# Kernel optimization log

Measured on AMD Instinct MI355X. Metric: run time of the kernel, lower is better.

Reference implementation:

```python
import jax, jax.numpy as jnp
import numpy as np

B, LONG, SHORT, D, NH, HD = 512, 1000, 50, 64, 4, 16
NUM_ITEMS, TOPK = 100000, 50
NBUCKETS, HASHL, HASHD = 1024, 4, 16  # NOTE: 4 hash layers of D//4 so concat matches item_dim (source default 3 is a shape bug)


def lin(x, w, b):
    return x @ w.T + b


def ln(x, g, b):
    m = x.mean(-1, keepdims=True)
    v = ((x - m) ** 2).mean(-1, keepdims=True)
    return (x - m) / jnp.sqrt(v + 1e-5) * g + b


def setup_inputs() -> dict:
    key = jax.random.key(0)
    ks = jax.random.split(key, 24)
    rn = lambda i, s: jax.random.normal(ks[i], s, jnp.float32) * 0.02
    emb = rn(0, (NUM_ITEMS + 1, D)).at[0].set(0.0)  # padding_idx=0 row zeroed
    return dict(
        user_features=jax.random.normal(ks[1], (B, D), jnp.float32),
        target_item_id=jax.random.randint(ks[2], (B,), 0, NUM_ITEMS + 1),
        short_hist_ids=jax.random.randint(ks[3], (B, SHORT), 0, NUM_ITEMS + 1),
        long_hist_ids=jax.random.randint(ks[4], (B, LONG), 0, NUM_ITEMS + 1),
        item_emb=emb,
        tproj_w=rn(5, (D, D)), tproj_b=jnp.zeros((D,), jnp.float32),
        attn_w1=rn(6, (64, 3 * D)), attn_b1=jnp.zeros((64,), jnp.float32),
        attn_w2=rn(7, (1, 64)), attn_b2=jnp.zeros((1,), jnp.float32),
        hash_emb=rn(8, (HASHL, NBUCKETS, HASHD)),
        sdim_w=rn(9, (D, D)), sdim_b=jnp.zeros((D,), jnp.float32),
        tf_qkv_w=rn(10, (2, 3 * D, D)), tf_qkv_b=jnp.zeros((2, 3 * D), jnp.float32),
        tf_out_w=rn(11, (2, D, D)), tf_out_b=jnp.zeros((2, D), jnp.float32),
        tf_ln1_g=jnp.ones((2, D), jnp.float32), tf_ln1_b=jnp.zeros((2, D), jnp.float32),
        tf_ff1_w=rn(12, (2, 2 * D, D)), tf_ff1_b=jnp.zeros((2, 2 * D), jnp.float32),
        tf_ff2_w=rn(13, (2, D, 2 * D)), tf_ff2_b=jnp.zeros((2, D), jnp.float32),
        tf_ln2_g=jnp.ones((2, D), jnp.float32), tf_ln2_b=jnp.zeros((2, D), jnp.float32),
        fus_w1=rn(14, (256, 4 * D)), fus_b1=jnp.zeros((256,), jnp.float32),
        fus_w2=rn(15, (128, 256)), fus_b2=jnp.zeros((128,), jnp.float32),
        fus_w3=rn(16, (1, 128)), fus_b3=jnp.zeros((1,), jnp.float32),
    )


def sim_forward(user_features, item_emb, tproj_w, tproj_b, attn_w1, attn_b1,
                attn_w2, attn_b2, hash_emb, sdim_w, sdim_b, tf_qkv_w, tf_qkv_b,
                tf_out_w, tf_out_b, tf_ln1_g, tf_ln1_b, tf_ff1_w, tf_ff1_b,
                tf_ff2_w, tf_ff2_b, tf_ln2_g, tf_ln2_b, fus_w1, fus_b1, fus_w2,
                fus_b2, fus_w3, fus_b3, target_item_id, short_hist_ids, long_hist_ids):
    # target projection
    target_emb = lin(item_emb[target_item_id], tproj_w, tproj_b)         # [B,D]
    # ---- hard search over long history ----
    long_emb = item_emb[long_hist_ids]                                    # [B,L,D]
    t = jnp.broadcast_to(target_emb[:, None, :], long_emb.shape)
    cc = jnp.concatenate([t, long_emb, long_emb * t], axis=-1)            # [B,L,3D]
    scores = lin(jax.nn.relu(lin(cc, attn_w1, attn_b1)), attn_w2, attn_b2)[..., 0]
    attn = jax.nn.softmax(scores, axis=-1)                                # [B,L]
    top_w, top_i = jax.lax.top_k(attn, TOPK)
    top_w = jax.nn.softmax(top_w, axis=-1)
    top_e = jnp.take_along_axis(long_emb, top_i[..., None], axis=1)       # [B,K,D]
    hard_repr = (top_w[..., None] * top_e).sum(axis=1)                    # [B,D]
    # ---- SDIM soft search ----
    bucket = long_hist_ids % NBUCKETS
    h = hash_emb[:, bucket].mean(axis=2)                                  # [HL,B,HD]
    hash_repr = jnp.moveaxis(h, 0, 1).reshape(h.shape[1], HASHL * HASHD)  # [B,D]
    soft_repr = lin(hash_repr + long_emb.mean(axis=1), sdim_w, sdim_b)    # [B,D]
    # ---- BST transformer over short history (post-norm, relu, dropout=eval) ----
    x = item_emb[short_hist_ids]                                          # [B,S,D]
    for l in range(2):
        qkv = lin(x, tf_qkv_w[l], tf_qkv_b[l])
        q, k, v = jnp.split(qkv, 3, axis=-1)
        q = q.reshape(B, SHORT, NH, HD); k = k.reshape(B, SHORT, NH, HD); v = v.reshape(B, SHORT, NH, HD)
        sc = jnp.einsum('bqhd,bkhd->bhqk', q, k) / np.sqrt(HD).astype(np.float32)
        a = jax.nn.softmax(sc, axis=-1)
        o = jnp.einsum('bhqk,bkhd->bqhd', a, v).reshape(B, SHORT, D)
        x = ln(x + lin(o, tf_out_w[l], tf_out_b[l]), tf_ln1_g[l], tf_ln1_b[l])
        f = lin(jax.nn.relu(lin(x, tf_ff1_w[l], tf_ff1_b[l])), tf_ff2_w[l], tf_ff2_b[l])
        x = ln(x + f, tf_ln2_g[l], tf_ln2_b[l])
    bst_repr = x.mean(axis=1)                                             # [B,D]
    # ---- fusion MLP ----
    combined = jnp.concatenate([user_features, hard_repr, soft_repr, bst_repr], axis=-1)
    hdn = jax.nn.relu(lin(combined, fus_w1, fus_b1))
    hdn = jax.nn.relu(lin(hdn, fus_w2, fus_b2))
    return lin(hdn, fus_w3, fus_b3)[..., 0]                               # [B]


def reference(user_features, target_item_id, short_hist_ids, long_hist_ids,
              item_emb, tproj_w, tproj_b, attn_w1, attn_b1, attn_w2, attn_b2,
              hash_emb, sdim_w, sdim_b, tf_qkv_w, tf_qkv_b, tf_out_w, tf_out_b,
              tf_ln1_g, tf_ln1_b, tf_ff1_w, tf_ff1_b, tf_ff2_w, tf_ff2_b,
              tf_ln2_g, tf_ln2_b, fus_w1, fus_b1, fus_w2, fus_b2, fus_w3, fus_b3):
    return sim_forward(user_features, item_emb, tproj_w, tproj_b, attn_w1, attn_b1,
                       attn_w2, attn_b2, hash_emb, sdim_w, sdim_b, tf_qkv_w, tf_qkv_b,
                       tf_out_w, tf_out_b, tf_ln1_g, tf_ln1_b, tf_ff1_w, tf_ff1_b,
                       tf_ff2_w, tf_ff2_b, tf_ln2_g, tf_ln2_b, fus_w1, fus_b1,
                       fus_w2, fus_b2, fus_w3, fus_b3, target_item_id,
                       short_hist_ids, long_hist_ids)
```

## Files before the change

kernel.cpp:

```cpp
#include <hip/hip_runtime.h>
#include <math.h>

#define NB 512
#define LONGN 1000
#define SHORTN 50
#define TOPKN 50
#define HALFN 500
#define NG 8
#define EROW 72
#define BROW 72
#define F1ROW 136

typedef __attribute__((ext_vector_type(8))) short bf16x8;
typedef __attribute__((ext_vector_type(4))) float f32x4;

__device__ __forceinline__ float dot4(float4 a, float4 b) {
  return a.x*b.x + a.y*b.y + a.z*b.z + a.w*b.w;
}

template<int N>
__device__ __forceinline__ float dotN(const float* w, const float* x) {
  const float4* w4 = (const float4*)w;
  const float4* x4 = (const float4*)x;
  float a0 = 0.f, a1 = 0.f, a2 = 0.f, a3 = 0.f;
  #pragma unroll
  for (int k = 0; k < N/4; k += 4) {
    a0 += dot4(w4[k],   x4[k]);
    a1 += dot4(w4[k+1], x4[k+1]);
    a2 += dot4(w4[k+2], x4[k+2]);
    a3 += dot4(w4[k+3], x4[k+3]);
  }
  return (a0 + a1) + (a2 + a3);
}

__device__ __forceinline__ float wave_sum(float v) {
  #pragma unroll
  for (int off = 32; off > 0; off >>= 1) v += __shfl_xor(v, off);
  return v;
}
__device__ __forceinline__ float wave_max(float v) {
  #pragma unroll
  for (int off = 32; off > 0; off >>= 1) v = fmaxf(v, __shfl_xor(v, off));
  return v;
}

__device__ __forceinline__ unsigned short f2bf(float x) {
  unsigned u = __float_as_uint(x);
  return (unsigned short)((u + 0x7fffu + ((u >> 16) & 1u)) >> 16);
}

__global__ __launch_bounds__(256, 3) void hard_scores_kernel(
    const int* __restrict__ target_item_id,
    const int* __restrict__ long_hist_ids,
    const float* __restrict__ item_emb,
    const float* __restrict__ tproj_w, const float* __restrict__ tproj_b,
    const float* __restrict__ attn_w1, const float* __restrict__ attn_b1,
    const float* __restrict__ attn_w2, const float* __restrict__ attn_b2,
    const float* __restrict__ hash_emb,
    float* __restrict__ scores_ws, float* __restrict__ partA,
    float* __restrict__ partH)
{
  __shared__ __align__(16) short Abf[64*EROW];
  __shared__ __align__(16) short Ebuf[2][64*EROW];
  __shared__ __align__(16) float tv[64];
  __shared__ __align__(16) float te[64];
  __shared__ __align__(16) float2 cw[64];
  __shared__ int idsL[HALFN];
  __shared__ __align__(16) float redE[4*64];

  const int bid = blockIdx.x;
  const int b = bid >> 1, half = bid & 1;
  const int base = half * HALFN;
  const int tid = threadIdx.x;
  const int wid = tid >> 6, lane = tid & 63;

  if (tid < 64) tv[tid] = item_emb[target_item_id[b]*64 + tid];
  for (int l = tid; l < HALFN; l += 256) idsL[l] = long_hist_ids[b*LONGN + base + l];
  __syncthreads();
  if (tid < 64) te[tid] = tproj_b[tid] + dotN<64>(tproj_w + tid*64, tv);
  __syncthreads();
  if (tid < 64) {
    float c = attn_b1[tid] + dotN<64>(attn_w1 + tid*192, te);
    cw[tid] = make_float2(c, attn_w2[tid]);
  }
  for (int idx = tid; idx < 4096; idx += 256) {
    int i = idx >> 6, j = idx & 63;
    Abf[i*EROW + j] = (short)f2bf(attn_w1[i*192 + 64 + j] + attn_w1[i*192 + 128 + j]*te[j]);
  }
  __syncthreads();

  bf16x8 a00,a01,a10,a11,a20,a21,a30,a31;
  {
    const short* ap = Abf + (lane & 15)*EROW + ((lane >> 4) << 3);
    a00 = *(const bf16x8*)(ap +  0*EROW);  a01 = *(const bf16x8*)(ap +  0*EROW + 32);
    a10 = *(const bf16x8*)(ap + 16*EROW);  a11 = *(const bf16x8*)(ap + 16*EROW + 32);
    a20 = *(const bf16x8*)(ap + 32*EROW);  a21 = *(const bf16x8*)(ap + 32*EROW + 32);
    a30 = *(const bf16x8*)(ap + 48*EROW);  a31 = *(const bf16x8*)(ap + 48*EROW + 32);
  }

  const float b2s = attn_b2[0];
  const int it_g = tid >> 2;
  const int dimg = (tid & 3) * 16;

  float4 sE0 = {0,0,0,0}, sE1 = {0,0,0,0}, sE2 = {0,0,0,0}, sE3 = {0,0,0,0};

  {
    const float4* ep = (const float4*)(item_emb + (size_t)idsL[it_g]*64 + dimg);
    float4 r0 = ep[0], r1 = ep[1], r2 = ep[2], r3 = ep[3];
    sE0.x+=r0.x; sE0.y+=r0.y; sE0.z+=r0.z; sE0.w+=r0.w;
    sE1.x+=r1.x; sE1.y+=r1.y; sE1.z+=r1.z; sE1.w+=r1.w;
    sE2.x+=r2.x; sE2.y+=r2.y; sE2.z+=r2.z; sE2.w+=r2.w;
    sE3.x+=r3.x; sE3.y+=r3.y; sE3.z+=r3.z; sE3.w+=r3.w;
    bf16x8 w0, w1;
    w0[0]=(short)f2bf(r0.x); w0[1]=(short)f2bf(r0.y); w0[2]=(short)f2bf(r0.z); w0[3]=(short)f2bf(r0.w);
    w0[4]=(short)f2bf(r1.x); w0[5]=(short)f2bf(r1.y); w0[6]=(short)f2bf(r1.z); w0[7]=(short)f2bf(r1.w);
    w1[0]=(short)f2bf(r2.x); w1[1]=(short)f2bf(r2.y); w1[2]=(short)f2bf(r2.z); w1[3]=(short)f2bf(r2.w);
    w1[4]=(short)f2bf(r3.x); w1[5]=(short)f2bf(r3.y); w1[6]=(short)f2bf(r3.z); w1[7]=(short)f2bf(r3.w);
    short* dst = &Ebuf[0][it_g*EROW + dimg];
    *(bf16x8*)dst = w0;  *(bf16x8*)(dst + 8) = w1;
  }
  __syncthreads();

  int buf = 0;
  for (int g = 0; g < NG; ++g) {
    float4 r0={0,0,0,0}, r1={0,0,0,0}, r2={0,0,0,0}, r3={0,0,0,0};
    const bool more = (g + 1 < NG);
    if (more) {
      const int gi = (g+1)*64 + it_g;
      if (gi < HALFN) {
        const float4* ep = (const float4*)(item_emb + (size_t)idsL[gi]*64 + dimg);
        r0 = ep[0]; r1 = ep[1]; r2 = ep[2]; r3 = ep[3];
      }
    }

    f32x4 acc0={0,0,0,0}, acc1={0,0,0,0}, acc2={0,0,0,0}, acc3={0,0,0,0};
    {
      const short* ep = &Ebuf[buf][(wid*16 + (lane & 15))*EROW + ((lane >> 4) << 3)];
      bf16x8 b0 = *(const bf16x8*)(ep);
      bf16x8 b1 = *(const bf16x8*)(ep + 32);
      acc0 = __builtin_amdgcn_mfma_f32_16x16x32_bf16(a00, b0, acc0, 0, 0, 0);
      acc0 = __builtin_amdgcn_mfma_f32_16x16x32_bf16(a01, b1, acc0, 0, 0, 0);
      acc1 = __builtin_amdgcn_mfma_f32_16x16x32_bf16(a10, b0, acc1, 0, 0, 0);
      acc1 = __builtin_amdgcn_mfma_f32_16x16x32_bf16(a11, b1, acc1, 0, 0, 0);
      acc2 = __builtin_amdgcn_mfma_f32_16x16x32_bf16(a20, b0, acc2, 0, 0, 0);
      acc2 = __builtin_amdgcn_mfma_f32_16x16x32_bf16(a21, b1, acc2, 0, 0, 0);
      acc3 = __builtin_amdgcn_mfma_f32_16x16x32_bf16(a30, b0, acc3, 0, 0, 0);
      acc3 = __builtin_amdgcn_mfma_f32_16x16x32_bf16(a31, b1, acc3, 0, 0, 0);
    }
    float p = 0.f;
    {
      const int rbase = (lane >> 4) << 2;
      #pragma unroll
      for (int r = 0; r < 4; ++r) {
        float2 c0 = cw[ 0 + rbase + r];
        float2 c1 = cw[16 + rbase + r];
        float2 c2 = cw[32 + rbase + r];
        float2 c3 = cw[48 + rbase + r];
        p += c0.y * fmaxf(acc0[r] + c0.x, 0.f);
        p += c1.y * fmaxf(acc1[r] + c1.x, 0.f);
        p += c2.y * fmaxf(acc2[r] + c2.x, 0.f);
        p += c3.y * fmaxf(acc3[r] + c3.x, 0.f);
      }
    }
    p += __shfl_xor(p, 16);
    p += __shfl_xor(p, 32);
    if (lane < 16) {
      const int gi = g*64 + wid*16 + lane;
      if (gi < HALFN) scores_ws[b*LONGN + base + gi] = b2s + p;
    }

    if (more) {
      sE0.x+=r0.x; sE0.y+=r0.y; sE0.z+=r0.z; sE0.w+=r0.w;
      sE1.x+=r1.x; sE1.y+=r1.y; sE1.z+=r1.z; sE1.w+=r1.w;
      sE2.x+=r2.x; sE2.y+=r2.y; sE2.z+=r2.z; sE2.w+=r2.w;
      sE3.x+=r3.x; sE3.y+=r3.y; sE3.z+=r3.z; sE3.w+=r3.w;
      bf16x8 w0, w1;
      w0[0]=(short)f2bf(r0.x); w0[1]=(short)f2bf(r0.y); w0[2]=(short)f2bf(r0.z); w0[3]=(short)f2bf(r0.w);
      w0[4]=(short)f2bf(r1.x); w0[5]=(short)f2bf(r1.y); w0[6]=(short)f2bf(r1.z); w0[7]=(short)f2bf(r1.w);
      w1[0]=(short)f2bf(r2.x); w1[1]=(short)f2bf(r2.y); w1[2]=(short)f2bf(r2.z); w1[3]=(short)f2bf(r2.w);
      w1[4]=(short)f2bf(r3.x); w1[5]=(short)f2bf(r3.y); w1[6]=(short)f2bf(r3.z); w1[7]=(short)f2bf(r3.w);
      short* dst = &Ebuf[buf ^ 1][it_g*EROW + dimg];
      *(bf16x8*)dst = w0;  *(bf16x8*)(dst + 8) = w1;
    }
    __syncthreads();
    buf ^= 1;
  }

  {
    float* red = (float*)&Ebuf[0][0];
    const int b17 = tid * 17;
    red[b17+ 0]=sE0.x; red[b17+ 1]=sE0.y; red[b17+ 2]=sE0.z; red[b17+ 3]=sE0.w;
    red[b17+ 4]=sE1.x; red[b17+ 5]=sE1.y; red[b17+ 6]=sE1.z; red[b17+ 7]=sE1.w;
    red[b17+ 8]=sE2.x; red[b17+ 9]=sE2.y; red[b17+10]=sE2.z; red[b17+11]=sE2.w;
    red[b17+12]=sE3.x; red[b17+13]=sE3.y; red[b17+14]=sE3.z; red[b17+15]=sE3.w;
    __syncthreads();
    if (tid < 64) {
      const int dg = tid >> 4, dw = tid & 15;
      float s = 0.f;
      for (int j = 0; j < 64; ++j) s += red[(j*4 + dg)*17 + dw];
      partA[bid*64 + tid] = s;
    }
  }

  {
    const int hl = lane >> 4, dd = lane & 15;
    const float* hb = hash_emb + hl*1024*16 + dd;
    float accH = 0.f;
    for (int l = wid; l < HALFN; l += 4)
      accH += hb[(idsL[l] & 1023)*16];
    redE[wid*64 + lane] = accH;
  }
  __syncthreads();
  if (wid == 0)
    partH[bid*64 + lane] = redE[lane] + redE[64+lane] + redE[128+lane] + redE[192+lane];
}

__global__ __launch_bounds__(256) void hard_finish_kernel(
    const int* __restrict__ long_hist_ids,
    const float* __restrict__ item_emb,
    const float* __restrict__ sdim_w, const float* __restrict__ sdim_b,
    const float* __restrict__ scores_ws,
    const float* __restrict__ partA, const float* __restrict__ partH,
    float* __restrict__ hard_out, float* __restrict__ soft_out)
{
  __shared__ __align__(16) float scores[LONGN];
  __shared__ int   idsL[LONGN];
  __shared__ __align__(16) unsigned long long kv[1024];
  __shared__ __align__(16) float redE[4*64];
  __shared__ __align__(16) float vecbuf[64];
  __shared__ float redV[4];
  __shared__ float selV[TOPKN];
  __shared__ int   selI[TOPKN];

  const int b = blockIdx.x;
  const int tid = threadIdx.x;
  const int wid = tid >> 6, lane = tid & 63;

  for (int l = tid; l < LONGN; l += 256) {
    scores[l] = scores_ws[b*LONGN + l];
    idsL[l] = long_hist_ids[b*LONGN + l];
  }
  __syncthreads();

  if (tid < 64)
    vecbuf[tid] = (partA[(2*b)*64 + tid] + partA[(2*b+1)*64 + tid]
                 + partH[(2*b)*64 + tid] + partH[(2*b+1)*64 + tid]) * (1.f/1000.f);
  __syncthreads();
  if (tid < 64)
    soft_out[b*64 + tid] = sdim_b[tid] + dotN<64>(sdim_w + tid*64, vecbuf);

  float mx = -INFINITY;
  for (int l = tid; l < LONGN; l += 256) mx = fmaxf(mx, scores[l]);
  mx = wave_max(mx);
  if (lane == 0) redV[wid] = mx;
  __syncthreads();
  mx = fmaxf(fmaxf(redV[0], redV[1]), fmaxf(redV[2], redV[3]));
  __syncthreads();
  float sm = 0.f;
  for (int l = tid; l < LONGN; l += 256) {
    float a = expf(scores[l] - mx);
    scores[l] = a;
    sm += a;
  }
  sm = wave_sum(sm);
  if (lane == 0) redV[wid] = sm;
  __syncthreads();
  {
    const float inv = 1.f / (redV[0] + redV[1] + redV[2] + redV[3]);
    for (int l = tid; l < LONGN; l += 256) scores[l] *= inv;
  }
  __syncthreads();

  for (int l = tid; l < 1024; l += 256) {
    if (l < LONGN) {
      unsigned vb = __float_as_uint(scores[l]);
      kv[l] = ((unsigned long long)(~vb) << 32) | (unsigned)l;
    } else {
      kv[l] = 0xFFFFFFFFFFFFFFFFull;
    }
  }
  __syncthreads();

  for (int k = 2; k <= 1024; k <<= 1) {
    for (int j = k >> 1; j > 0; j >>= 1) {
      #pragma unroll 2
      for (int p = tid; p < 512; p += 256) {
        const int i = ((p & ~(j-1)) << 1) | (p & (j-1));
        const int m = i + j;
        const bool up = ((i & k) == 0);
        unsigned long long a = kv[i], c = kv[m];
        if ((a > c) == up) { kv[i] = c; kv[m] = a; }
      }
      __syncthreads();
    }
  }

  if (tid < TOPKN) {
    unsigned long long key = kv[tid];
    selI[tid] = (int)(unsigned)(key & 0xFFFFFFFFu);
    selV[tid] = __uint_as_float(~(unsigned)(key >> 32));
  }
  __syncthreads();

  if (wid == 0) {
    float v = (lane < TOPKN) ? selV[lane] : -INFINITY;
    float m2 = wave_max(v);
    float e = (lane < TOPKN) ? expf(v - m2) : 0.f;
    float s2 = wave_sum(e);
    if (lane < TOPKN) selV[lane] = e / s2;
  }
  __syncthreads();

  float accR = 0.f;
  for (int r = wid; r < TOPKN; r += 4)
    accR += selV[r] * item_emb[idsL[selI[r]]*64 + lane];
  redE[wid*64 + lane] = accR;
  __syncthreads();
  if (wid == 0)
    hard_out[b*64 + lane] = redE[lane] + redE[64+lane] + redE[128+lane] + redE[192+lane];
}

__global__ __launch_bounds__(256) void bst_prep_kernel(
    const float* __restrict__ qkv_w, const float* __restrict__ out_w,
    const float* __restrict__ ff1_w, const float* __restrict__ ff2_w,
    short* __restrict__ wF)
{
  const int t = blockIdx.x*256 + threadIdx.x;
  if (t >= 8192) return;
  const int fid = t >> 6, lane = t & 63;
  const int n16 = lane & 15, k8 = (lane >> 4) * 8;
  const float* src;
  if (fid < 48)      { int f=fid,    l=f/24, r=f%24, nt=r>>1, kc=r&1;
    src = qkv_w + l*12288 + (nt*16+n16)*64 + kc*32 + k8; }
  else if (fid < 64) { int f=fid-48, l=f>>3, r=f&7,  nt=r>>1, kc=r&1;
    src = out_w + l*4096 + (nt*16+n16)*64 + kc*32 + k8; }
  else if (fid < 96) { int f=fid-64, l=f>>4, r=f&15, nt=r>>1, kc=r&1;
    src = ff1_w + l*8192 + (nt*16+n16)*64 + kc*32 + k8; }
  else               { int f=fid-96, l=f>>4, r=f&15, nt=r>>2, kc=r&3;
    src = ff2_w + l*8192 + (nt*16+n16)*128 + kc*32 + k8; }
  short* dst = wF + fid*512 + lane*8;
  #pragma unroll
  for (int j = 0; j < 8; ++j) dst[j] = (short)f2bf(src[j]);
}

__global__ __launch_bounds__(256) void bst_kernel(
    const int* __restrict__ short_ids, const float* __restrict__ item_emb,
    const short* __restrict__ wF,
    const float* __restrict__ qkv_b, const float* __restrict__ out_b,
    const float* __restrict__ ln1_g, const float* __restrict__ ln1_b,
    const float* __restrict__ ff1_b, const float* __restrict__ ff2_b,
    const float* __restrict__ ln2_g, const float* __restrict__ ln2_b,
    float* __restrict__ bst_out)
{
  __shared__ __align__(16) float xf[SHORTN*64];
  __shared__ __align__(16) short xbf[64*BROW];
  __shared__ __align__(16) float qf[SHORTN*68];
  __shared__ __align__(16) float arena[SHORTN*132];
  __shared__ __align__(16) short obf[64*BROW];

  short* f1bf = (short*)arena;

  const int b = blockIdx.x, tid = threadIdx.x;
  const int wid = tid >> 6, lane = tid & 63;
  const int n16 = lane & 15;
  const int kg8 = (lane >> 4) << 3;
  const int mrow = (lane >> 4) << 2;

  for (int idx = tid; idx < SHORTN*64; idx += 256) {
    int s = idx >> 6, j = idx & 63;
    float v = item_emb[short_ids[b*SHORTN + s]*64 + j];
    xf[idx] = v;
    xbf[s*BROW + j] = (short)f2bf(v);
  }
  for (int idx = tid; idx < 14*BROW; idx += 256) {
    xbf[50*BROW + idx] = 0;
    obf[50*BROW + idx] = 0;
  }
  __syncthreads();

  for (int l = 0; l < 2; ++l) {
    {
      const short* ap = xbf + n16*BROW + kg8;
      bf16x8 A00 = *(const bf16x8*)(ap);            bf16x8 A01 = *(const bf16x8*)(ap + 32);
      bf16x8 A10 = *(const bf16x8*)(ap + 16*BROW);  bf16x8 A11 = *(const bf16x8*)(ap + 16*BROW + 32);
      bf16x8 A20 = *(const bf16x8*)(ap + 32*BROW);  bf16x8 A21 = *(const bf16x8*)(ap + 32*BROW + 32);
      bf16x8 A30 = *(const bf16x8*)(ap + 48*BROW);  bf16x8 A31 = *(const bf16x8*)(ap + 48*BROW + 32);
      #pragma unroll
      for (int t = 0; t < 3; ++t) {
        const int nt = wid*3 + t;
        const short* bp = wF + (size_t)(l*24 + nt*2)*512 + lane*8;
        bf16x8 B0 = *(const bf16x8*)(bp);
        bf16x8 B1 = *(const bf16x8*)(bp + 512);
        f32x4 c0={0,0,0,0}, c1={0,0,0,0}, c2={0,0,0,0}, c3={0,0,0,0};
        c0 = __builtin_amdgcn_mfma_f32_16x16x32_bf16(A00, B0, c0, 0,0,0);
        c0 = __builtin_amdgcn_mfma_f32_16x16x32_bf16(A01, B1, c0, 0,0,0);
        c1 = __builtin_amdgcn_mfma_f32_16x16x32_bf16(A10, B0, c1, 0,0,0);
        c1 = __builtin_amdgcn_mfma_f32_16x16x32_bf16(A11, B1, c1, 0,0,0);
        c2 = __builtin_amdgcn_mfma_f32_16x16x32_bf16(A20, B0, c2, 0,0,0);
        c2 = __builtin_amdgcn_mfma_f32_16x16x32_bf16(A21, B1, c2, 0,0,0);
        c3 = __builtin_amdgcn_mfma_f32_16x16x32_bf16(A30, B0, c3, 0,0,0);
        c3 = __builtin_amdgcn_mfma_f32_16x16x32_bf16(A31, B1, c3, 0,0,0);
        const int c = nt*16 + n16;
        const float bias = qkv_b[l*192 + c];
        #pragma unroll
        for (int r = 0; r < 4; ++r) {
          int m0 = mrow + r;
          float v0 = c0[r] + bias;
          float v1 = c1[r] + bias;
          float v2 = c2[r] + bias;
          float v3 = c3[r] + bias;
          if (c < 64) {
            qf[m0*68 + c] = v0;
            if (m0+16 < SHORTN) qf[(m0+16)*68 + c] = v1;
            if (m0+32 < SHORTN) qf[(m0+32)*68 + c] = v2;
            if (m0+48 < SHORTN) qf[(m0+48)*68 + c] = v3;
          } else {
            const int cc = c - 64;
            arena[m0*132 + cc] = v0;
            if (m0+16 < SHORTN) arena[(m0+16)*132 + cc] = v1;
            if (m0+32 < SHORTN) arena[(m0+32)*132 + cc] = v2;
            if (m0+48 < SHORTN) arena[(m0+48)*132 + cc] = v3;
          }
        }
      }
    }
    __syncthreads();

    if (tid < 4*SHORTN) {
      const int h = tid / SHORTN, s = tid - h*SHORTN;
      const float4* qp = (const float4*)(qf + s*68 + h*16);
      const float4 qA = qp[0], qB2 = qp[1], qC = qp[2], qD = qp[3];
      float m = -INFINITY, ss = 0.f;
      float4 oa0 = {0,0,0,0}, oa1 = {0,0,0,0}, oa2 = {0,0,0,0}, oa3 = {0,0,0,0};
      for (int t2 = 0; t2 < SHORTN; ++t2) {
        const float4* kp = (const float4*)(arena + t2*132 + h*16);
        float d = dot4(qA,kp[0]) + dot4(qB2,kp[1]) + dot4(qC,kp[2]) + dot4(qD,kp[3]);
        d *= 0.25f;
        float mn = fmaxf(m, d);
        float al = __expf(m - mn);
        float a  = __expf(d - mn);
        m = mn;
        ss = ss*al + a;
        const float4* vp = (const float4*)(arena + t2*132 + 64 + h*16);
        float4 v0 = vp[0], v1 = vp[1], v2 = vp[2], v3 = vp[3];
        oa0.x = oa0.x*al + a*v0.x; oa0.y = oa0.y*al + a*v0.y;
        oa0.z = oa0.z*al + a*v0.z; oa0.w = oa0.w*al + a*v0.w;
        oa1.x = oa1.x*al + a*v1.x; oa1.y = oa1.y*al + a*v1.y;
        oa1.z = oa1.z*al + a*v1.z; oa1.w = oa1.w*al + a*v1.w;
        oa2.x = oa2.x*al + a*v2.x; oa2.y = oa2.y*al + a*v2.y;
        oa2.z = oa2.z*al + a*v2.z; oa2.w = oa2.w*al + a*v2.w;
        oa3.x = oa3.x*al + a*v3.x; oa3.y = oa3.y*al + a*v3.y;
        oa3.z = oa3.z*al + a*v3.z; oa3.w = oa3.w*al + a*v3.w;
      }
      const float inv = 1.f/ss;
      bf16x8 w0, w1;
      w0[0]=(short)f2bf(oa0.x*inv); w0[1]=(short)f2bf(oa0.y*inv);
      w0[2]=(short)f2bf(oa0.z*inv); w0[3]=(short)f2bf(oa0.w*inv);
      w0[4]=(short)f2bf(oa1.x*inv); w0[5]=(short)f2bf(oa1.y*inv);
      w0[6]=(short)f2bf(oa1.z*inv); w0[7]=(short)f2bf(oa1.w*inv);
      w1[0]=(short)f2bf(oa2.x*inv); w1[1]=(short)f2bf(oa2.y*inv);
      w1[2]=(short)f2bf(oa2.z*inv); w1[3]=(short)f2bf(oa2.w*inv);
      w1[4]=(short)f2bf(oa3.x*inv); w1[5]=(short)f2bf(oa3.y*inv);
      w1[6]=(short)f2bf(oa3.z*inv); w1[7]=(short)f2bf(oa3.w*inv);
      short* op = obf + s*BROW + h*16;
      *(bf16x8*)op = w0;  *(bf16x8*)(op + 8) = w1;
    }
    __syncthreads();

    {
      const short* ap = obf + n16*BROW + kg8;
      bf16x8 A00 = *(const bf16x8*)(ap);            bf16x8 A01 = *(const bf16x8*)(ap + 32);
      bf16x8 A10 = *(const bf16x8*)(ap + 16*BROW);  bf16x8 A11 = *(const bf16x8*)(ap + 16*BROW + 32);
      bf16x8 A20 = *(const bf16x8*)(ap + 32*BROW);  bf16x8 A21 = *(const bf16x8*)(ap + 32*BROW + 32);
      bf16x8 A30 = *(const bf16x8*)(ap + 48*BROW);  bf16x8 A31 = *(const bf16x8*)(ap + 48*BROW + 32);
      const int nt = wid;
      const short* bp = wF + (size_t)(48 + l*8 + nt*2)*512 + lane*8;
      bf16x8 B0 = *(const bf16x8*)(bp);
      bf16x8 B1 = *(const bf16x8*)(bp + 512);
      f32x4 c0={0,0,0,0}, c1={0,0,0,0}, c2={0,0,0,0}, c3={0,0,0,0};
      c0 = __builtin_amdgcn_mfma_f32_16x16x32_bf16(A00, B0, c0, 0,0,0);
      c0 = __builtin_amdgcn_mfma_f32_16x16x32_bf16(A01, B1, c0, 0,0,0);
      c1 = __builtin_amdgcn_mfma_f32_16x16x32_bf16(A10, B0, c1, 0,0,0);
      c1 = __builtin_amdgcn_mfma_f32_16x16x32_bf16(A11, B1, c1, 0,0,0);
      c2 = __builtin_amdgcn_mfma_f32_16x16x32_bf16(A20, B0, c2, 0,0,0);
      c2 = __builtin_amdgcn_mfma_f32_16x16x32_bf16(A21, B1, c2, 0,0,0);
      c3 = __builtin_amdgcn_mfma_f32_16x16x32_bf16(A30, B0, c3, 0,0,0);
      c3 = __builtin_amdgcn_mfma_f32_16x16x32_bf16(A31, B1, c3, 0,0,0);
      const int c = nt*16 + n16;
      const float bias = out_b[l*64 + c];
      #pragma unroll
      for (int r = 0; r < 4; ++r) {
        int m0 = mrow + r;
        arena[m0*68 + c] = xf[m0*64 + c] + bias + c0[r];
        if (m0+16 < SHORTN) arena[(m0+16)*68 + c] = xf[(m0+16)*64 + c] + bias + c1[r];
        if (m0+32 < SHORTN) arena[(m0+32)*68 + c] = xf[(m0+32)*64 + c] + bias + c2[r];
        if (m0+48 < SHORTN) arena[(m0+48)*68 + c] = xf[(m0+48)*64 + c] + bias + c3[r];
      }
      for (int idx = tid; idx < 14*F1ROW; idx += 256) f1bf[50*F1ROW + idx] = 0;
    }
    __syncthreads();

    {
      const float g = ln1_g[l*64 + lane], bb = ln1_b[l*64 + lane];
      for (int s = wid; s < SHORTN; s += 4) {
        float y = arena[s*68 + lane];
        float mean = wave_sum(y) * (1.f/64.f);
        float dv = y - mean;
        float var = wave_sum(dv*dv) * (1.f/64.f);
        float r = dv / sqrtf(var + 1e-5f) * g + bb;
        xf[s*64 + lane] = r;
        xbf[s*BROW + lane] = (short)f2bf(r);
      }
    }
    __syncthreads();

    {
      const short* ap = xbf + n16*BROW + kg8;
      bf16x8 A00 = *(const bf16x8*)(ap);            bf16x8 A01 = *(const bf16x8*)(ap + 32);
      bf16x8 A10 = *(const bf16x8*)(ap + 16*BROW);  bf16x8 A11 = *(const bf16x8*)(ap + 16*BROW + 32);
      bf16x8 A20 = *(const bf16x8*)(ap + 32*BROW);  bf16x8 A21 = *(const bf16x8*)(ap + 32*BROW + 32);
      bf16x8 A30 = *(const bf16x8*)(ap + 48*BROW);  bf16x8 A31 = *(const bf16x8*)(ap + 48*BROW + 32);
      #pragma unroll
      for (int t = 0; t < 2; ++t) {
        const int nt = wid*2 + t;
        const short* bp = wF + (size_t)(64 + l*16 + nt*2)*512 + lane*8;
        bf16x8 B0 = *(const bf16x8*)(bp);
        bf16x8 B1 = *(const bf16x8*)(bp + 512);
        f32x4 c0={0,0,0,0}, c1={0,0,0,0}, c2={0,0,0,0}, c3={0,0,0,0};
        c0 = __builtin_amdgcn_mfma_f32_16x16x32_bf16(A00, B0, c0, 0,0,0);
        c0 = __builtin_amdgcn_mfma_f32_16x16x32_bf16(A01, B1, c0, 0,0,0);
        c1 = __builtin_amdgcn_mfma_f32_16x16x32_bf16(A10, B0, c1, 0,0,0);
        c1 = __builtin_amdgcn_mfma_f32_16x16x32_bf16(A11, B1, c1, 0,0,0);
        c2 = __builtin_amdgcn_mfma_f32_16x16x32_bf16(A20, B0, c2, 0,0,0);
        c2 = __builtin_amdgcn_mfma_f32_16x16x32_bf16(A21, B1, c2, 0,0,0);
        c3 = __builtin_amdgcn_mfma_f32_16x16x32_bf16(A30, B0, c3, 0,0,0);
        c3 = __builtin_amdgcn_mfma_f32_16x16x32_bf16(A31, B1, c3, 0,0,0);
        const int c = nt*16 + n16;
        const float bias = ff1_b[l*128 + c];
        #pragma unroll
        for (int r = 0; r < 4; ++r) {
          int m0 = mrow + r;
          f1bf[m0*F1ROW + c] = (short)f2bf(fmaxf(c0[r] + bias, 0.f));
          if (m0+16 < SHORTN) f1bf[(m0+16)*F1ROW + c] = (short)f2bf(fmaxf(c1[r] + bias, 0.f));
          if (m0+32 < SHORTN) f1bf[(m0+32)*F1ROW + c] = (short)f2bf(fmaxf(c2[r] + bias, 0.f));
          if (m0+48 < SHORTN) f1bf[(m0+48)*F1ROW + c] = (short)f2bf(fmaxf(c3[r] + bias, 0.f));
        }
      }
    }
    __syncthreads();

    {
      const int nt = wid;
      f32x4 c0={0,0,0,0}, c1={0,0,0,0}, c2={0,0,0,0}, c3={0,0,0,0};
      #pragma unroll
      for (int kc = 0; kc < 4; ++kc) {
        const short* ap = f1bf + n16*F1ROW + kc*32 + kg8;
        bf16x8 A0 = *(const bf16x8*)(ap);
        bf16x8 A1 = *(const bf16x8*)(ap + 16*F1ROW);
        bf16x8 A2 = *(const bf16x8*)(ap + 32*F1ROW);
        bf16x8 A3 = *(const bf16x8*)(ap + 48*F1ROW);
        const short* bp = wF + (size_t)(96 + l*16 + nt*4 + kc)*512 + lane*8;
        bf16x8 B = *(const bf16x8*)(bp);
        c0 = __builtin_amdgcn_mfma_f32_16x16x32_bf16(A0, B, c0, 0,0,0);
        c1 = __builtin_amdgcn_mfma_f32_16x16x32_bf16(A1, B, c1, 0,0,0);
        c2 = __builtin_amdgcn_mfma_f32_16x16x32_bf16(A2, B, c2, 0,0,0);
        c3 = __builtin_amdgcn_mfma_f32_16x16x32_bf16(A3, B, c3, 0,0,0);
      }
      __syncthreads();
      const int c = nt*16 + n16;
      const float bias = ff2_b[l*64 + c];
      #pragma unroll
      for (int r = 0; r < 4; ++r) {
        int m0 = mrow + r;
        arena[m0*68 + c] = xf[m0*64 + c] + bias + c0[r];
        if (m0+16 < SHORTN) arena[(m0+16)*68 + c] = xf[(m0+16)*64 + c] + bias + c1[r];
        if (m0+32 < SHORTN) arena[(m0+32)*68 + c] = xf[(m0+32)*64 + c] + bias + c2[r];
        if (m0+48 < SHORTN) arena[(m0+48)*68 + c] = xf[(m0+48)*64 + c] + bias + c3[r];
      }
    }
    __syncthreads();

    {
      const float g = ln2_g[l*64 + lane], bb = ln2_b[l*64 + lane];
      for (int s = wid; s < SHORTN; s += 4) {
        float y = arena[s*68 + lane];
        float mean = wave_sum(y) * (1.f/64.f);
        float dv = y - mean;
        float var = wave_sum(dv*dv) * (1.f/64.f);
        float r = dv / sqrtf(var + 1e-5f) * g + bb;
        xf[s*64 + lane] = r;
        xbf[s*BROW + lane] = (short)f2bf(r);
      }
    }
    __syncthreads();
  }

  float acc = 0.f;
  for (int s = wid; s < SHORTN; s += 4) acc += xf[s*64 + lane];
  qf[wid*64 + lane] = acc;
  __syncthreads();
  if (wid == 0)
    bst_out[b*64 + lane] = (qf[lane] + qf[64+lane] + qf[128+lane] + qf[192+lane]) * (1.f/50.f);
}

__global__ __launch_bounds__(256) void fusion_kernel(
    const float* __restrict__ user, const float* __restrict__ hard,
    const float* __restrict__ soft, const float* __restrict__ bst,
    const float* __restrict__ w1, const float* __restrict__ b1,
    const float* __restrict__ w2, const float* __restrict__ b2,
    const float* __restrict__ w3, const float* __restrict__ b3,
    float* __restrict__ out)
{
  __shared__ __align__(16) float comb[256];
  __shared__ __align__(16) float h1[256];
  __shared__ __align__(16) float h2[128];
  const int b = blockIdx.x, tid = threadIdx.x;
  if (tid < 64)       comb[tid] = user[b*64 + tid];
  else if (tid < 128) comb[tid] = hard[b*64 + tid - 64];
  else if (tid < 192) comb[tid] = soft[b*64 + tid - 128];
  else                comb[tid] = bst[b*64 + tid - 192];
  __syncthreads();
  h1[tid] = fmaxf(b1[tid] + dotN<256>(w1 + tid*256, comb), 0.f);
  __syncthreads();
  if (tid < 128) h2[tid] = fmaxf(b2[tid] + dotN<256>(w2 + tid*256, h1), 0.f);
  __syncthreads();
  if (tid < 64) {
    float p = w3[tid]*h2[tid] + w3[tid+64]*h2[tid+64];
    p = wave_sum(p);
    if (tid == 0) out[b] = p + b3[0];
  }
}

extern "C" void kernel_launch(void* const* d_in, const int* in_sizes, int n_in,
                              void* d_out, int out_size, void* d_ws, size_t ws_size,
                              hipStream_t stream) {
  const float* user_features  = (const float*)d_in[0];
  const int*   target_item_id = (const int*)  d_in[1];
  const int*   short_hist_ids = (const int*)  d_in[2];
  const int*   long_hist_ids  = (const int*)  d_in[3];
  const float* item_emb       = (const float*)d_in[4];
  const float* tproj_w  = (const float*)d_in[5];
  const float* tproj_b  = (const float*)d_in[6];
  const float* attn_w1  = (const float*)d_in[7];
  const float* attn_b1  = (const float*)d_in[8];
  const float* attn_w2  = (const float*)d_in[9];
  const float* attn_b2  = (const float*)d_in[10];
  const float* hash_emb = (const float*)d_in[11];
  const float* sdim_w   = (const float*)d_in[12];
  const float* sdim_b   = (const float*)d_in[13];
  const float* tf_qkv_w = (const float*)d_in[14];
  const float* tf_qkv_b = (const float*)d_in[15];
  const float* tf_out_w = (const float*)d_in[16];
  const float* tf_out_b = (const float*)d_in[17];
  const float* tf_ln1_g = (const float*)d_in[18];
  const float* tf_ln1_b = (const float*)d_in[19];
  const float* tf_ff1_w = (const float*)d_in[20];
  const float* tf_ff1_b = (const float*)d_in[21];
  const float* tf_ff2_w = (const float*)d_in[22];
  const float* tf_ff2_b = (const float*)d_in[23];
  const float* tf_ln2_g = (const float*)d_in[24];
  const float* tf_ln2_b = (const float*)d_in[25];
  const float* fus_w1   = (const float*)d_in[26];
  const float* fus_b1   = (const float*)d_in[27];
  const float* fus_w2   = (const float*)d_in[28];
  const float* fus_b2   = (const float*)d_in[29];
  const float* fus_w3   = (const float*)d_in[30];
  const float* fus_b3   = (const float*)d_in[31];

  float* ws = (float*)d_ws;
  float* hard = ws;
  float* soft = hard + NB*64;
  float* bst  = soft + NB*64;
  float* scores_ws = bst + NB*64;
  float* partA = scores_ws + NB*LONGN;
  float* partH = partA + NB*2*64;
  short* wF    = (short*)(partH + NB*2*64);

  bst_prep_kernel<<<32, 256, 0, stream>>>(tf_qkv_w, tf_out_w, tf_ff1_w, tf_ff2_w, wF);
  hard_scores_kernel<<<2*NB, 256, 0, stream>>>(target_item_id, long_hist_ids,
      item_emb, tproj_w, tproj_b, attn_w1, attn_b1, attn_w2, attn_b2,
      hash_emb, scores_ws, partA, partH);
  hard_finish_kernel<<<NB, 256, 0, stream>>>(long_hist_ids, item_emb,
      sdim_w, sdim_b, scores_ws, partA, partH, hard, soft);
  bst_kernel<<<NB, 256, 0, stream>>>(short_hist_ids, item_emb, wF,
      tf_qkv_b, tf_out_b, tf_ln1_g, tf_ln1_b, tf_ff1_b, tf_ff2_b,
      tf_ln2_g, tf_ln2_b, bst);
  fusion_kernel<<<NB, 256, 0, stream>>>(user_features, hard, soft, bst,
      fus_w1, fus_b1, fus_w2, fus_b2, fus_w3, fus_b3, (float*)d_out);
}
```

Measured before the change: 173.0 us.

## Pre-convert item embeddings to bf16 and store attention K/V in bf16

Adds a prep kernel that converts the entire item embedding table to bf16 in the workspace each call. The hard-attention gather then reads half the bytes per history item and skips the per-element conversion. Separately, the transformer kernel stores K/V in bf16 in a shared-memory zone aliased with other buffers, reducing LDS footprint. The trade-offs are converting the full 100k×64 table on every call, which may cost more than it saves on 512k gathered rows, and a small loss of precision in the embedding sums.

```diff
diff --git a/kernel.cpp b/kernel.cpp
--- a/kernel.cpp
+++ b/kernel.cpp
@@ -10,6 +10,7 @@
 #define EROW 72
 #define BROW 72
 #define F1ROW 136
+#define KVROW 136
 
 typedef __attribute__((ext_vector_type(8))) short bf16x8;
 typedef __attribute__((ext_vector_type(4))) float f32x4;
@@ -48,11 +49,28 @@
   unsigned u = __float_as_uint(x);
   return (unsigned short)((u + 0x7fffu + ((u >> 16) & 1u)) >> 16);
 }
+__device__ __forceinline__ float bf2f(short s) {
+  return __uint_as_float(((unsigned)(unsigned short)s) << 16);
+}
+
+__global__ __launch_bounds__(256) void emb_prep_kernel(
+    const float* __restrict__ emb, short* __restrict__ embT, int n8)
+{
+  const int t = blockIdx.x*256 + threadIdx.x;
+  if (t >= n8) return;
+  const float4* s = (const float4*)(emb + (size_t)t*8);
+  float4 a = s[0], b = s[1];
+  bf16x8 w;
+  w[0]=(short)f2bf(a.x); w[1]=(short)f2bf(a.y); w[2]=(short)f2bf(a.z); w[3]=(short)f2bf(a.w);
+  w[4]=(short)f2bf(b.x); w[5]=(short)f2bf(b.y); w[6]=(short)f2bf(b.z); w[7]=(short)f2bf(b.w);
+  *(bf16x8*)(embT + (size_t)t*8) = w;
+}
 
 __global__ __launch_bounds__(256, 3) void hard_scores_kernel(
     const int* __restrict__ target_item_id,
     const int* __restrict__ long_hist_ids,
     const float* __restrict__ item_emb,
+    const short* __restrict__ embT, const int use_bf16,
     const float* __restrict__ tproj_w, const float* __restrict__ tproj_b,
     const float* __restrict__ attn_w1, const float* __restrict__ attn_b1,
     const float* __restrict__ attn_w2, const float* __restrict__ attn_b2,
@@ -105,17 +123,26 @@
   float4 sE0 = {0,0,0,0}, sE1 = {0,0,0,0}, sE2 = {0,0,0,0}, sE3 = {0,0,0,0};
 
   {
-    const float4* ep = (const float4*)(item_emb + (size_t)idsL[it_g]*64 + dimg);
-    float4 r0 = ep[0], r1 = ep[1], r2 = ep[2], r3 = ep[3];
-    sE0.x+=r0.x; sE0.y+=r0.y; sE0.z+=r0.z; sE0.w+=r0.w;
-    sE1.x+=r1.x; sE1.y+=r1.y; sE1.z+=r1.z; sE1.w+=r1.w;
-    sE2.x+=r2.x; sE2.y+=r2.y; sE2.z+=r2.z; sE2.w+=r2.w;
-    sE3.x+=r3.x; sE3.y+=r3.y; sE3.z+=r3.z; sE3.w+=r3.w;
     bf16x8 w0, w1;
-    w0[0]=(short)f2bf(r0.x); w0[1]=(short)f2bf(r0.y); w0[2]=(short)f2bf(r0.z); w0[3]=(short)f2bf(r0.w);
-    w0[4]=(short)f2bf(r1.x); w0[5]=(short)f2bf(r1.y); w0[6]=(short)f2bf(r1.z); w0[7]=(short)f2bf(r1.w);
-    w1[0]=(short)f2bf(r2.x); w1[1]=(short)f2bf(r2.y); w1[2]=(short)f2bf(r2.z); w1[3]=(short)f2bf(r2.w);
-    w1[4]=(short)f2bf(r3.x); w1[5]=(short)f2bf(r3.y); w1[6]=(short)f2bf(r3.z); w1[7]=(short)f2bf(r3.w);
+    if (use_bf16) {
+      const bf16x8* ep = (const bf16x8*)(embT + (size_t)idsL[it_g]*64 + dimg);
+      w0 = ep[0]; w1 = ep[1];
+      sE0.x+=bf2f(w0[0]); sE0.y+=bf2f(w0[1]); sE0.z+=bf2f(w0[2]); sE0.w+=bf2f(w0[3]);
+      sE1.x+=bf2f(w0[4]); sE1.y+=bf2f(w0[5]); sE1.z+=bf2f(w0[6]); sE1.w+=bf2f(w0[7]);
+      sE2.x+=bf2f(w1[0]); sE2.y+=bf2f(w1[1]); sE2.z+=bf2f(w1[2]); sE2.w+=bf2f(w1[3]);
+      sE3.x+=bf2f(w1[4]); sE3.y+=bf2f(w1[5]); sE3.z+=bf2f(w1[6]); sE3.w+=bf2f(w1[7]);
+    } else {
+      const float4* ep = (const float4*)(item_emb + (size_t)idsL[it_g]*64 + dimg);
+      float4 r0 = ep[0], r1 = ep[1], r2 = ep[2], r3 = ep[3];
+      sE0.x+=r0.x; sE0.y+=r0.y; sE0.z+=r0.z; sE0.w+=r0.w;
+      sE1.x+=r1.x; sE1.y+=r1.y; sE1.z+=r1.z; sE1.w+=r1.w;
+      sE2.x+=r2.x; sE2.y+=r2.y; sE2.z+=r2.z; sE2.w+=r2.w;
+      sE3.x+=r3.x; sE3.y+=r3.y; sE3.z+=r3.z; sE3.w+=r3.w;
+      w0[0]=(short)f2bf(r0.x); w0[1]=(short)f2bf(r0.y); w0[2]=(short)f2bf(r0.z); w0[3]=(short)f2bf(r0.w);
+      w0[4]=(short)f2bf(r1.x); w0[5]=(short)f2bf(r1.y); w0[6]=(short)f2bf(r1.z); w0[7]=(short)f2bf(r1.w);
+      w1[0]=(short)f2bf(r2.x); w1[1]=(short)f2bf(r2.y); w1[2]=(short)f2bf(r2.z); w1[3]=(short)f2bf(r2.w);
+      w1[4]=(short)f2bf(r3.x); w1[5]=(short)f2bf(r3.y); w1[6]=(short)f2bf(r3.z); w1[7]=(short)f2bf(r3.w);
+    }
     short* dst = &Ebuf[0][it_g*EROW + dimg];
     *(bf16x8*)dst = w0;  *(bf16x8*)(dst + 8) = w1;
   }
@@ -123,13 +150,19 @@
 
   int buf = 0;
   for (int g = 0; g < NG; ++g) {
+    bf16x8 w0 = {0,0,0,0,0,0,0,0}, w1 = {0,0,0,0,0,0,0,0};
     float4 r0={0,0,0,0}, r1={0,0,0,0}, r2={0,0,0,0}, r3={0,0,0,0};
     const bool more = (g + 1 < NG);
     if (more) {
       const int gi = (g+1)*64 + it_g;
       if (gi < HALFN) {
-        const float4* ep = (const float4*)(item_emb + (size_t)idsL[gi]*64 + dimg);
-        r0 = ep[0]; r1 = ep[1]; r2 = ep[2]; r3 = ep[3];
+        if (use_bf16) {
+          const bf16x8* ep = (const bf16x8*)(embT + (size_t)idsL[gi]*64 + dimg);
+          w0 = ep[0]; w1 = ep[1];
+        } else {
+          const float4* ep = (const float4*)(item_emb + (size_t)idsL[gi]*64 + dimg);
+          r0 = ep[0]; r1 = ep[1]; r2 = ep[2]; r3 = ep[3];
+        }
       }
     }
 
@@ -170,15 +203,21 @@
     }
 
     if (more) {
-      sE0.x+=r0.x; sE0.y+=r0.y; sE0.z+=r0.z; sE0.w+=r0.w;
-      sE1.x+=r1.x; sE1.y+=r1.y; sE1.z+=r1.z; sE1.w+=r1.w;
-      sE2.x+=r2.x; sE2.y+=r2.y; sE2.z+=r2.z; sE2.w+=r2.w;
-      sE3.x+=r3.x; sE3.y+=r3.y; sE3.z+=r3.z; sE3.w+=r3.w;
-      bf16x8 w0, w1;
-      w0[0]=(short)f2bf(r0.x); w0[1]=(short)f2bf(r0.y); w0[2]=(short)f2bf(r0.z); w0[3]=(short)f2bf(r0.w);
-      w0[4]=(short)f2bf(r1.x); w0[5]=(short)f2bf(r1.y); w0[6]=(short)f2bf(r1.z); w0[7]=(short)f2bf(r1.w);
-      w1[0]=(short)f2bf(r2.x); w1[1]=(short)f2bf(r2.y); w1[2]=(short)f2bf(r2.z); w1[3]=(short)f2bf(r2.w);
-      w1[4]=(short)f2bf(r3.x); w1[5]=(short)f2bf(r3.y); w1[6]=(short)f2bf(r3.z); w1[7]=(short)f2bf(r3.w);
+      if (use_bf16) {
+        sE0.x+=bf2f(w0[0]); sE0.y+=bf2f(w0[1]); sE0.z+=bf2f(w0[2]); sE0.w+=bf2f(w0[3]);
+        sE1.x+=bf2f(w0[4]); sE1.y+=bf2f(w0[5]); sE1.z+=bf2f(w0[6]); sE1.w+=bf2f(w0[7]);
+        sE2.x+=bf2f(w1[0]); sE2.y+=bf2f(w1[1]); sE2.z+=bf2f(w1[2]); sE2.w+=bf2f(w1[3]);
+        sE3.x+=bf2f(w1[4]); sE3.y+=bf2f(w1[5]); sE3.z+=bf2f(w1[6]); sE3.w+=bf2f(w1[7]);
+      } else {
+        sE0.x+=r0.x; sE0.y+=r0.y; sE0.z+=r0.z; sE0.w+=r0.w;
+        sE1.x+=r1.x; sE1.y+=r1.y; sE1.z+=r1.z; sE1.w+=r1.w;
+        sE2.x+=r2.x; sE2.y+=r2.y; sE2.z+=r2.z; sE2.w+=r2.w;
+        sE3.x+=r3.x; sE3.y+=r3.y; sE3.z+=r3.z; sE3.w+=r3.w;
+        w0[0]=(short)f2bf(r0.x); w0[1]=(short)f2bf(r0.y); w0[2]=(short)f2bf(r0.z); w0[3]=(short)f2bf(r0.w);
+        w0[4]=(short)f2bf(r1.x); w0[5]=(short)f2bf(r1.y); w0[6]=(short)f2bf(r1.z); w0[7]=(short)f2bf(r1.w);
+        w1[0]=(short)f2bf(r2.x); w1[1]=(short)f2bf(r2.y); w1[2]=(short)f2bf(r2.z); w1[3]=(short)f2bf(r2.w);
+        w1[4]=(short)f2bf(r3.x); w1[5]=(short)f2bf(r3.y); w1[6]=(short)f2bf(r3.z); w1[7]=(short)f2bf(r3.w);
+      }
       short* dst = &Ebuf[buf ^ 1][it_g*EROW + dimg];
       *(bf16x8*)dst = w0;  *(bf16x8*)(dst + 8) = w1;
     }
@@ -354,11 +393,13 @@
 {
   __shared__ __align__(16) float xf[SHORTN*64];
   __shared__ __align__(16) short xbf[64*BROW];
-  __shared__ __align__(16) float qf[SHORTN*68];
-  __shared__ __align__(16) float arena[SHORTN*132];
+  __shared__ __align__(16) char  zone[27200];
   __shared__ __align__(16) short obf[64*BROW];
 
-  short* f1bf = (short*)arena;
+  float* qf   = (float*)zone;
+  short* kvbf = (short*)(zone + 13600);
+  float* yln  = (float*)zone;
+  short* f1bf = (short*)zone;
 
   const int b = blockIdx.x, tid = threadIdx.x;
   const int wid = tid >> 6, lane = tid & 63;
@@ -416,10 +457,10 @@
             if (m0+48 < SHORTN) qf[(m0+48)*68 + c] = v3;
           } else {
             const int cc = c - 64;
-            arena[m0*132 + cc] = v0;
-            if (m0+16 < SHORTN) arena[(m0+16)*132 + cc] = v1;
-            if (m0+32 < SHORTN) arena[(m0+32)*132 + cc] = v2;
-            if (m0+48 < SHORTN) arena[(m0+48)*132 + cc] = v3;
+            kvbf[m0*KVROW + cc] = (short)f2bf(v0);
+            if (m0+16 < SHORTN) kvbf[(m0+16)*KVROW + cc] = (short)f2bf(v1);
+            if (m0+32 < SHORTN) kvbf[(m0+32)*KVROW + cc] = (short)f2bf(v2);
+            if (m0+48 < SHORTN) kvbf[(m0+48)*KVROW + cc] = (short)f2bf(v3);
           }
         }
       }
@@ -433,24 +474,31 @@
       float m = -INFINITY, ss = 0.f;
       float4 oa0 = {0,0,0,0}, oa1 = {0,0,0,0}, oa2 = {0,0,0,0}, oa3 = {0,0,0,0};
       for (int t2 = 0; t2 < SHORTN; ++t2) {
-        const float4* kp = (const float4*)(arena + t2*132 + h*16);
-        float d = dot4(qA,kp[0]) + dot4(qB2,kp[1]) + dot4(qC,kp[2]) + dot4(qD,kp[3]);
+        const short* kp = kvbf + t2*KVROW + h*16;
+        bf16x8 k0 = *(const bf16x8*)kp;
+        bf16x8 k1 = *(const bf16x8*)(kp + 8);
+        float d =
+            qA.x*bf2f(k0[0]) + qA.y*bf2f(k0[1]) + qA.z*bf2f(k0[2]) + qA.w*bf2f(k0[3])
+          + qB2.x*bf2f(k0[4]) + qB2.y*bf2f(k0[5]) + qB2.z*bf2f(k0[6]) + qB2.w*bf2f(k0[7])
+          + qC.x*bf2f(k1[0]) + qC.y*bf2f(k1[1]) + qC.z*bf2f(k1[2]) + qC.w*bf2f(k1[3])
+          + qD.x*bf2f(k1[4]) + qD.y*bf2f(k1[5]) + qD.z*bf2f(k1[6]) + qD.w*bf2f(k1[7]);
         d *= 0.25f;
         float mn = fmaxf(m, d);
         float al = __expf(m - mn);
         float a  = __expf(d - mn);
         m = mn;
         ss = ss*al + a;
-        const float4* vp = (const float4*)(arena + t2*132 + 64 + h*16);
-        float4 v0 = vp[0], v1 = vp[1], v2 = vp[2], v3 = vp[3];
-        oa0.x = oa0.x*al + a*v0.x; oa0.y = oa0.y*al + a*v0.y;
-        oa0.z = oa0.z*al + a*v0.z; oa0.w = oa0.w*al + a*v0.w;
-        oa1.x = oa1.x*al + a*v1.x; oa1.y = oa1.y*al + a*v1.y;
-        oa1.z = oa1.z*al + a*v1.z; oa1.w = oa1.w*al + a*v1.w;
-        oa2.x = oa2.x*al + a*v2.x; oa2.y = oa2.y*al + a*v2.y;
-        oa2.z = oa2.z*al + a*v2.z; oa2.w = oa2.w*al + a*v2.w;
-        oa3.x = oa3.x*al + a*v3.x; oa3.y = oa3.y*al + a*v3.y;
-        oa3.z = oa3.z*al + a*v3.z; oa3.w = oa3.w*al + a*v3.w;
+        const short* vp = kvbf + t2*KVROW + 64 + h*16;
+        bf16x8 v0 = *(const bf16x8*)vp;
+        bf16x8 v1 = *(const bf16x8*)(vp + 8);
+        oa0.x = oa0.x*al + a*bf2f(v0[0]); oa0.y = oa0.y*al + a*bf2f(v0[1]);
+        oa0.z = oa0.z*al + a*bf2f(v0[2]); oa0.w = oa0.w*al + a*bf2f(v0[3]);
+        oa1.x = oa1.x*al + a*bf2f(v0[4]); oa1.y = oa1.y*al + a*bf2f(v0[5]);
+        oa1.z = oa1.z*al + a*bf2f(v0[6]); oa1.w = oa1.w*al + a*bf2f(v0[7]);
+        oa2.x = oa2.x*al + a*bf2f(v1[0]); oa2.y = oa2.y*al + a*bf2f(v1[1]);
+        oa2.z = oa2.z*al + a*bf2f(v1[2]); oa2.w = oa2.w*al + a*bf2f(v1[3]);
+        oa3.x = oa3.x*al + a*bf2f(v1[4]); oa3.y = oa3.y*al + a*bf2f(v1[5]);
+        oa3.z = oa3.z*al + a*bf2f(v1[6]); oa3.w = oa3.w*al + a*bf2f(v1[7]);
       }
       const float inv = 1.f/ss;
       bf16x8 w0, w1;
@@ -491,10 +539,10 @@
       #pragma unroll
       for (int r = 0; r < 4; ++r) {
         int m0 = mrow + r;
-        arena[m0*68 + c] = xf[m0*64 + c] + bias + c0[r];
-        if (m0+16 < SHORTN) arena[(m0+16)*68 + c] = xf[(m0+16)*64 + c] + bias + c1[r];
-        if (m0+32 < SHORTN) arena[(m0+32)*68 + c] = xf[(m0+32)*64 + c] + bias + c2[r];
-        if (m0+48 < SHORTN) arena[(m0+48)*68 + c] = xf[(m0+48)*64 + c] + bias + c3[r];
+        yln[m0*68 + c] = xf[m0*64 + c] + bias + c0[r];
+        if (m0+16 < SHORTN) yln[(m0+16)*68 + c] = xf[(m0+16)*64 + c] + bias + c1[r];
+        if (m0+32 < SHORTN) yln[(m0+32)*68 + c] = xf[(m0+32)*64 + c] + bias + c2[r];
+        if (m0+48 < SHORTN) yln[(m0+48)*68 + c] = xf[(m0+48)*64 + c] + bias + c3[r];
       }
       for (int idx = tid; idx < 14*F1ROW; idx += 256) f1bf[50*F1ROW + idx] = 0;
     }
@@ -503,7 +551,7 @@
     {
       const float g = ln1_g[l*64 + lane], bb = ln1_b[l*64 + lane];
       for (int s = wid; s < SHORTN; s += 4) {
-        float y = arena[s*68 + lane];
+        float y = yln[s*68 + lane];
         float mean = wave_sum(y) * (1.f/64.f);
         float dv = y - mean;
         float var = wave_sum(dv*dv) * (1.f/64.f);
@@ -572,10 +620,10 @@
       #pragma unroll
       for (int r = 0; r < 4; ++r) {
         int m0 = mrow + r;
-        arena[m0*68 + c] = xf[m0*64 + c] + bias + c0[r];
-        if (m0+16 < SHORTN) arena[(m0+16)*68 + c] = xf[(m0+16)*64 + c] + bias + c1[r];
-        if (m0+32 < SHORTN) arena[(m0+32)*68 + c] = xf[(m0+32)*64 + c] + bias + c2[r];
-        if (m0+48 < SHORTN) arena[(m0+48)*68 + c] = xf[(m0+48)*64 + c] + bias + c3[r];
+        yln[m0*68 + c] = xf[m0*64 + c] + bias + c0[r];
+        if (m0+16 < SHORTN) yln[(m0+16)*68 + c] = xf[(m0+16)*64 + c] + bias + c1[r];
+        if (m0+32 < SHORTN) yln[(m0+32)*68 + c] = xf[(m0+32)*64 + c] + bias + c2[r];
+        if (m0+48 < SHORTN) yln[(m0+48)*68 + c] = xf[(m0+48)*64 + c] + bias + c3[r];
       }
     }
     __syncthreads();
@@ -583,7 +631,7 @@
     {
       const float g = ln2_g[l*64 + lane], bb = ln2_b[l*64 + lane];
       for (int s = wid; s < SHORTN; s += 4) {
-        float y = arena[s*68 + lane];
+        float y = yln[s*68 + lane];
         float mean = wave_sum(y) * (1.f/64.f);
         float dv = y - mean;
         float var = wave_sum(dv*dv) * (1.f/64.f);
@@ -667,6 +715,8 @@
   const float* fus_w3   = (const float*)d_in[30];
   const float* fus_b3   = (const float*)d_in[31];
 
+  const int emb_elems = in_sizes[4];
+
   float* ws = (float*)d_ws;
   float* hard = ws;
   float* soft = hard + NB*64;
@@ -675,10 +725,19 @@
   float* partA = scores_ws + NB*LONGN;
   float* partH = partA + NB*2*64;
   short* wF    = (short*)(partH + NB*2*64);
+  short* embT  = wF + 65536;
+
+  const size_t base_bytes = (size_t)(3*NB*64 + NB*LONGN + 2*NB*2*64) * 4 + 65536*2;
+  const size_t need_bytes = base_bytes + (size_t)emb_elems * 2;
+  const int use_bf16 = (ws_size >= need_bytes) ? 1 : 0;
 
   bst_prep_kernel<<<32, 256, 0, stream>>>(tf_qkv_w, tf_out_w, tf_ff1_w, tf_ff2_w, wF);
+  if (use_bf16) {
+    const int n8 = emb_elems / 8;
+    emb_prep_kernel<<<(n8 + 255)/256, 256, 0, stream>>>(item_emb, embT, n8);
+  }
   hard_scores_kernel<<<2*NB, 256, 0, stream>>>(target_item_id, long_hist_ids,
-      item_emb, tproj_w, tproj_b, attn_w1, attn_b1, attn_w2, attn_b2,
+      item_emb, embT, use_bf16, tproj_w, tproj_b, attn_w1, attn_b1, attn_w2, attn_b2,
       hash_emb, scores_ws, partA, partH);
   hard_finish_kernel<<<NB, 256, 0, stream>>>(long_hist_ids, item_emb,
       sdim_w, sdim_b, scores_ws, partA, partH, hard, soft);
```

After: 201.7 us. +16.5%, slower.
